# Performance work log

Hardware: AMD Instinct MI355X
Metric: run time of the kernel (lower is better)

Reference implementation:

```python
import jax, jax.numpy as jnp
import numpy as np

B, M, N, D, C = 4, 256, 64, 512, 1024  # batch, frames, tokens, d_model, n_classes


def setup_inputs() -> dict:
    key = jax.random.key(0)
    ks = jax.random.split(key, 6)
    s = 1.0 / np.sqrt(D)
    return {
        "encoder_out": jax.random.normal(ks[0], (B, M, D), jnp.float32),
        "decoder_out": jax.random.normal(ks[1], (B, N, D), jnp.float32),
        "W1": jax.random.normal(ks[2], (D, 2 * D), jnp.float32) * s,  # torch Linear [out,in], in=joint_size=2*d_model
        "b1": jax.random.normal(ks[3], (D,), jnp.float32) * s,
        "W2": jax.random.normal(ks[4], (C, D), jnp.float32) * s,
        "b2": jax.random.normal(ks[5], (C,), jnp.float32) * s,
    }


def reference(encoder_out, decoder_out, W1, b1, W2, b2):
    # cat([enc, dec], -1) @ W1.T == enc @ W1[:, :D].T + dec @ W1[:, D:].T
    # so project each side separately, then broadcast-add (avoids the [B,M,N,2D] concat).
    d = encoder_out.shape[-1]
    proj_enc = jnp.einsum("bmd,kd->bmk", encoder_out, W1[:, :d])   # [B,M,D]
    proj_dec = jnp.einsum("bnd,kd->bnk", decoder_out, W1[:, d:])   # [B,N,D]
    hidden = jnp.tanh(proj_enc[:, :, None, :] + proj_dec[:, None, :, :] + b1)  # [B,M,N,D]
    logits = jnp.einsum("bmnd,cd->bmnc", hidden, W2) + b2          # [B,M,N,C]
    return jax.nn.log_softmax(logits, axis=-1)
```

## Files before the change

kernel.cpp:

```cpp
#include <hip/hip_runtime.h>
#include <hip/hip_bf16.h>
#include <stdint.h>


typedef __bf16         bf16x8 __attribute__((ext_vector_type(8)));
typedef float          f32x4  __attribute__((ext_vector_type(4)));
typedef float          f32x16 __attribute__((ext_vector_type(16)));
typedef unsigned short u16x8  __attribute__((ext_vector_type(8)));

__device__ __forceinline__ unsigned short f2bf(float f) {
  unsigned int u = __float_as_uint(f);
  u += 0x7fffu + ((u >> 16) & 1u);
  return (unsigned short)(u >> 16);
}

__device__ __forceinline__ f32x4 mfma16(u16x8 a, u16x8 b, f32x4 c) {
  return __builtin_amdgcn_mfma_f32_16x16x32_bf16(
      __builtin_bit_cast(bf16x8, a), __builtin_bit_cast(bf16x8, b), c, 0, 0, 0);
}
__device__ __forceinline__ f32x16 mfma32(u16x8 a, u16x8 b, f32x16 c) {
  return __builtin_amdgcn_mfma_f32_32x32x16_bf16(
      __builtin_bit_cast(bf16x8, a), __builtin_bit_cast(bf16x8, b), c, 0, 0, 0);
}

__device__ __forceinline__ void stage16(const void* g, void* l) {
  __builtin_amdgcn_global_load_lds(
      (const __attribute__((address_space(1))) void*)g,
      (__attribute__((address_space(3))) void*)l, 16, 0, 0);
}

__global__ __launch_bounds__(256) void prep_kernel(
    const float* __restrict__ enc, const float* __restrict__ dec,
    const float* __restrict__ W1,  const float* __restrict__ W2,
    unsigned short* __restrict__ encB, unsigned short* __restrict__ decB,
    unsigned short* __restrict__ W1eB, unsigned short* __restrict__ W1dB,
    unsigned short* __restrict__ W2t)
{
  const int i = blockIdx.x * 256 + threadIdx.x;
  encB[i] = f2bf(enc[i]);
  {
    const int e  = i & 7;
    const int l  = (i >> 3) & 63;
    const int cb = (i >> 9) & 1;
    const int ks = (i >> 10) & 31;
    const int w  = i >> 15;
    const int col = w * 64 + cb * 32 + (l & 31);
    const int k   = ks * 16 + (l >> 5) * 8 + e;
    W2t[i] = f2bf(W2[col * 512 + k]);
  }
  if (i < 262144) {
    const int k = i >> 9, d = i & 511;
    W1eB[i] = f2bf(W1[k * 1024 + d]);
    W1dB[i] = f2bf(W1[k * 1024 + 512 + d]);
  }
  if (i < 131072) decB[i] = f2bf(dec[i]);
}

__global__ __launch_bounds__(256) void proj_kernel(
    const unsigned short* __restrict__ encB, const unsigned short* __restrict__ decB,
    const unsigned short* __restrict__ W1eB, const unsigned short* __restrict__ W1dB,
    const float* __restrict__ b1, float* __restrict__ pe, float* __restrict__ pd)
{
  int bid = blockIdx.x;
  const unsigned short *A, *Wt;
  const float* bias;
  float* out;
  if (bid < 128) { A = encB; Wt = W1eB; bias = nullptr; out = pe; }
  else           { bid -= 128; A = decB; Wt = W1dB; bias = b1; out = pd; }
  const int rtile = bid >> 3;
  const int ctile = bid & 7;
  const int w = threadIdx.x >> 6;
  const int l = threadIdx.x & 63;
  const int q = l >> 4, ln = l & 15;

  f32x4 acc[4] = {};
  const unsigned short* Ab = A  + (size_t)(rtile * 64 + ln) * 512 + q * 8;
  const unsigned short* Wb = Wt + (size_t)(ctile * 64 + w * 16 + ln) * 512 + q * 8;

#pragma unroll 4
  for (int ks = 0; ks < 16; ++ks) {
    u16x8 bv = *(const u16x8*)(Wb + ks * 32);
#pragma unroll
    for (int rf = 0; rf < 4; ++rf) {
      u16x8 av = *(const u16x8*)(Ab + rf * 16 * 512 + ks * 32);
      acc[rf] = mfma16(av, bv, acc[rf]);
    }
  }
  const int col = ctile * 64 + w * 16 + ln;
  const float bv = bias ? bias[col] : 0.0f;
#pragma unroll
  for (int rf = 0; rf < 4; ++rf)
#pragma unroll
    for (int j = 0; j < 4; ++j)
      out[(size_t)(rtile * 64 + rf * 16 + q * 4 + j) * 512 + col] = acc[rf][j] + bv;
}

__global__ __launch_bounds__(1024) void joint_kernel(
    const float* __restrict__ pe, const float* __restrict__ pd,
    const unsigned short* __restrict__ W2t, const float* __restrict__ b2,
    float* __restrict__ out)
{
  __shared__ unsigned short A_sh[64 * 512];
  __shared__ unsigned short B_sh[16 * 2048];
  __shared__ float red[64][17];
  __shared__ float lse_sh[64];

  const int blk = blockIdx.x;
  const int b   = blk >> 8;
  const int tid = threadIdx.x;
  const int w = tid >> 6, l = tid & 63;
  const int lo = l & 31, hi = l >> 5;

  const unsigned short* Wsrc = W2t + (size_t)w * 32768;
  unsigned short* Bdst = B_sh + w * 2048;

  stage16(Wsrc + l * 8,       Bdst);
  stage16(Wsrc + 512 + l * 8, Bdst + 512);

  float b2v[2];
#pragma unroll
  for (int cb = 0; cb < 2; ++cb) b2v[cb] = b2[w * 64 + cb * 32 + lo];
  asm volatile("" :: "v"(b2v[0]), "v"(b2v[1]));

  {
    const float* per = pe + (size_t)blk * 512 + l * 8;
    const float4 pe0 = *(const float4*)(per);
    const float4 pe1 = *(const float4*)(per + 4);
#pragma unroll
    for (int r = 0; r < 4; ++r) {
      const int n = (w << 2) | r;
      const float* pdr = pd + (size_t)((b << 6) | n) * 512 + l * 8;
      const float4 q0 = *(const float4*)(pdr);
      const float4 q1 = *(const float4*)(pdr + 4);
      float x[8] = {pe0.x + q0.x, pe0.y + q0.y, pe0.z + q0.z, pe0.w + q0.w,
                    pe1.x + q1.x, pe1.y + q1.y, pe1.z + q1.z, pe1.w + q1.w};
      u16x8 pk;
#pragma unroll
      for (int e = 0; e < 8; ++e) {
        const float ex = __expf(2.0f * x[e]);
        const float tv = 1.0f - 2.0f * __builtin_amdgcn_rcpf(ex + 1.0f);
        pk[e] = f2bf(tv);
      }
      *(u16x8*)((char*)A_sh + n * 1024 + ((l ^ (n & 7)) << 4)) = pk;
    }
  }
  __syncthreads();

  f32x16 acc[2][2];
#pragma unroll
  for (int rb = 0; rb < 2; ++rb)
#pragma unroll
    for (int cb = 0; cb < 2; ++cb) acc[rb][cb] = (f32x16)(0.f);

  const char* Abase = (const char*)A_sh + lo * 1024;
  const int x7 = lo & 7;
  const unsigned short* Bread = B_sh + w * 2048 + l * 8;

#pragma unroll
  for (int ks = 0; ks < 32; ++ks) {
    __builtin_amdgcn_sched_barrier(0);
    if (ks < 31) {
      stage16(Wsrc + (ks + 1) * 1024 + l * 8,       Bdst + ((ks + 1) & 1) * 1024);
      stage16(Wsrc + (ks + 1) * 1024 + 512 + l * 8, Bdst + ((ks + 1) & 1) * 1024 + 512);
      __builtin_amdgcn_sched_barrier(0);
      asm volatile("s_waitcnt vmcnt(2)" ::: "memory");
    } else {
      asm volatile("s_waitcnt vmcnt(0)" ::: "memory");
    }
    __builtin_amdgcn_sched_barrier(0);

    u16x8 bv[2], av[2];
#pragma unroll
    for (int cb = 0; cb < 2; ++cb)
      bv[cb] = *(const u16x8*)(Bread + (ks & 1) * 1024 + cb * 512);
#pragma unroll
    for (int rb = 0; rb < 2; ++rb)
      av[rb] = *(const u16x8*)(Abase + rb * 32768 + (((2 * ks + hi) ^ x7) << 4));
#pragma unroll
    for (int rb = 0; rb < 2; ++rb)
#pragma unroll
      for (int cb = 0; cb < 2; ++cb)
        acc[rb][cb] = mfma32(av[rb], bv[cb], acc[rb][cb]);
  }

  const float L2E = 1.4426950408889634f;
  const float LN2 = 0.6931471805599453f;

#pragma unroll
  for (int rb = 0; rb < 2; ++rb) {
    float s[16];
#pragma unroll
    for (int reg = 0; reg < 16; ++reg) {
      const float x0 = acc[rb][0][reg] + b2v[0];
      const float x1 = acc[rb][1][reg] + b2v[1];
      acc[rb][0][reg] = x0;
      acc[rb][1][reg] = x1;
      s[reg] = __builtin_amdgcn_exp2f(x0 * L2E) + __builtin_amdgcn_exp2f(x1 * L2E);
    }
#pragma unroll
    for (int o = 1; o < 32; o <<= 1)
#pragma unroll
      for (int reg = 0; reg < 16; ++reg)
        s[reg] += __shfl_xor(s[reg], o);
    if (lo == 0) {
#pragma unroll
      for (int reg = 0; reg < 16; ++reg) {
        const int row = rb * 32 + (reg & 3) + 8 * (reg >> 2) + 4 * hi;
        red[row][w] = s[reg];
      }
    }
  }
  __syncthreads();

  if (tid < 64) {
    float s = red[tid][0];
#pragma unroll
    for (int ww = 1; ww < 16; ++ww) s += red[tid][ww];
    lse_sh[tid] = LN2 * __builtin_amdgcn_logf(s);
  }
  __syncthreads();

  float* outb = out + (size_t)blk * 65536 + w * 64 + lo;
#pragma unroll
  for (int rb = 0; rb < 2; ++rb)
#pragma unroll
    for (int reg = 0; reg < 16; ++reg) {
      const int row = rb * 32 + (reg & 3) + 8 * (reg >> 2) + 4 * hi;
      const float lse = lse_sh[row];
      float* orow = outb + (size_t)row * 1024;
      orow[0]  = acc[rb][0][reg] - lse;
      orow[32] = acc[rb][1][reg] - lse;
    }
}

extern "C" void kernel_launch(void* const* d_in, const int* in_sizes, int n_in,
                              void* d_out, int out_size, void* d_ws, size_t ws_size,
                              hipStream_t stream) {
  (void)in_sizes; (void)n_in; (void)out_size; (void)ws_size;
  const float* enc = (const float*)d_in[0];
  const float* dec = (const float*)d_in[1];
  const float* W1  = (const float*)d_in[2];
  const float* b1  = (const float*)d_in[3];
  const float* W2  = (const float*)d_in[4];
  const float* b2  = (const float*)d_in[5];
  float* out = (float*)d_out;

  char* ws = (char*)d_ws;
  unsigned short* encB = (unsigned short*)(ws + 0);
  unsigned short* decB = (unsigned short*)(ws + 1048576);
  unsigned short* W1eB = (unsigned short*)(ws + 1310720);
  unsigned short* W1dB = (unsigned short*)(ws + 1835008);
  unsigned short* W2t  = (unsigned short*)(ws + 2359296);
  float*          pe   = (float*)(ws + 3407872);
  float*          pd   = (float*)(ws + 5505024);

  prep_kernel<<<2048, 256, 0, stream>>>(enc, dec, W1, W2, encB, decB, W1eB, W1dB, W2t);
  proj_kernel<<<160, 256, 0, stream>>>(encB, decB, W1eB, W1dB, b1, pe, pd);
  joint_kernel<<<1024, 1024, 0, stream>>>(pe, pd, W2t, b2, out);
}
```

Baseline: 152.0 us.

## Fuse bf16 prep conversion into projection kernel and drop intermediate buffers

Merges the prep and projection kernels into one launch. Projection blocks now read fp32 encoder, decoder and W1 directly and convert to bf16 in registers. Extra blocks in the same grid build the W2 transposed bf16 layout. This removes one kernel launch and the round trip through bf16 copies of enc, dec and W1. In exchange the projection reads twice the bytes per operand and repeats the conversion per tile, and the fp32 loads are less vectorized.

```diff
diff --git a/kernel.cpp b/kernel.cpp
--- a/kernel.cpp
+++ b/kernel.cpp
@@ -14,6 +14,15 @@
   return (unsigned short)(u >> 16);
 }
 
+__device__ __forceinline__ u16x8 cvt8(const float* p) {
+  const float4 a = *(const float4*)p;
+  const float4 b = *(const float4*)(p + 4);
+  u16x8 r;
+  r[0] = f2bf(a.x); r[1] = f2bf(a.y); r[2] = f2bf(a.z); r[3] = f2bf(a.w);
+  r[4] = f2bf(b.x); r[5] = f2bf(b.y); r[6] = f2bf(b.z); r[7] = f2bf(b.w);
+  return r;
+}
+
 __device__ __forceinline__ f32x4 mfma16(u16x8 a, u16x8 b, f32x4 c) {
   return __builtin_amdgcn_mfma_f32_16x16x32_bf16(
       __builtin_bit_cast(bf16x8, a), __builtin_bit_cast(bf16x8, b), c, 0, 0, 0);
@@ -29,60 +38,52 @@
       (__attribute__((address_space(3))) void*)l, 16, 0, 0);
 }
 
-__global__ __launch_bounds__(256) void prep_kernel(
+__global__ __launch_bounds__(256) void prep_proj_kernel(
     const float* __restrict__ enc, const float* __restrict__ dec,
     const float* __restrict__ W1,  const float* __restrict__ W2,
-    unsigned short* __restrict__ encB, unsigned short* __restrict__ decB,
-    unsigned short* __restrict__ W1eB, unsigned short* __restrict__ W1dB,
-    unsigned short* __restrict__ W2t)
+    const float* __restrict__ b1,
+    unsigned short* __restrict__ W2t, float* __restrict__ pe, float* __restrict__ pd)
 {
-  const int i = blockIdx.x * 256 + threadIdx.x;
-  encB[i] = f2bf(enc[i]);
-  {
-    const int e  = i & 7;
-    const int l  = (i >> 3) & 63;
-    const int cb = (i >> 9) & 1;
-    const int ks = (i >> 10) & 31;
-    const int w  = i >> 15;
-    const int col = w * 64 + cb * 32 + (l & 31);
-    const int k   = ks * 16 + (l >> 5) * 8 + e;
-    W2t[i] = f2bf(W2[col * 512 + k]);
-  }
-  if (i < 262144) {
-    const int k = i >> 9, d = i & 511;
-    W1eB[i] = f2bf(W1[k * 1024 + d]);
-    W1dB[i] = f2bf(W1[k * 1024 + 512 + d]);
-  }
-  if (i < 131072) decB[i] = f2bf(dec[i]);
-}
-
-__global__ __launch_bounds__(256) void proj_kernel(
-    const unsigned short* __restrict__ encB, const unsigned short* __restrict__ decB,
-    const unsigned short* __restrict__ W1eB, const unsigned short* __restrict__ W1dB,
-    const float* __restrict__ b1, float* __restrict__ pe, float* __restrict__ pd)
-{
-  int bid = blockIdx.x;
-  const unsigned short *A, *Wt;
+  const int bid = blockIdx.x;
+  if (bid >= 160) {
+    const int base = (bid - 160) * 4096;
+#pragma unroll
+    for (int j = 0; j < 16; ++j) {
+      const int i = base + j * 256 + threadIdx.x;
+      const int e  = i & 7;
+      const int l  = (i >> 3) & 63;
+      const int cb = (i >> 9) & 1;
+      const int ks = (i >> 10) & 31;
+      const int w  = i >> 15;
+      const int col = w * 64 + cb * 32 + (l & 31);
+      const int k   = ks * 16 + (l >> 5) * 8 + e;
+      W2t[i] = f2bf(W2[col * 512 + k]);
+    }
+    return;
+  }
+
+  int pb = bid;
+  const float* Af;
   const float* bias;
-  float* out;
-  if (bid < 128) { A = encB; Wt = W1eB; bias = nullptr; out = pe; }
-  else           { bid -= 128; A = decB; Wt = W1dB; bias = b1; out = pd; }
-  const int rtile = bid >> 3;
-  const int ctile = bid & 7;
+  float* outp;
+  int woff;
+  if (pb < 128) { Af = enc; bias = nullptr; outp = pe; woff = 0; }
+  else { pb -= 128; Af = dec; bias = b1; outp = pd; woff = 512; }
+  const int rtile = pb >> 3;
+  const int ctile = pb & 7;
   const int w = threadIdx.x >> 6;
   const int l = threadIdx.x & 63;
   const int q = l >> 4, ln = l & 15;
 
   f32x4 acc[4] = {};
-  const unsigned short* Ab = A  + (size_t)(rtile * 64 + ln) * 512 + q * 8;
-  const unsigned short* Wb = Wt + (size_t)(ctile * 64 + w * 16 + ln) * 512 + q * 8;
-
-#pragma unroll 4
+  const float* Ab = Af + (size_t)(rtile * 64 + ln) * 512 + q * 8;
+  const float* Wb = W1 + (size_t)(ctile * 64 + w * 16 + ln) * 1024 + woff + q * 8;
+
   for (int ks = 0; ks < 16; ++ks) {
-    u16x8 bv = *(const u16x8*)(Wb + ks * 32);
+    u16x8 bv = cvt8(Wb + ks * 32);
 #pragma unroll
     for (int rf = 0; rf < 4; ++rf) {
-      u16x8 av = *(const u16x8*)(Ab + rf * 16 * 512 + ks * 32);
+      u16x8 av = cvt8(Ab + rf * 16 * 512 + ks * 32);
       acc[rf] = mfma16(av, bv, acc[rf]);
     }
   }
@@ -92,7 +93,7 @@
   for (int rf = 0; rf < 4; ++rf)
 #pragma unroll
     for (int j = 0; j < 4; ++j)
-      out[(size_t)(rtile * 64 + rf * 16 + q * 4 + j) * 512 + col] = acc[rf][j] + bv;
+      outp[(size_t)(rtile * 64 + rf * 16 + q * 4 + j) * 512 + col] = acc[rf][j] + bv;
 }
 
 __global__ __launch_bounds__(1024) void joint_kernel(
@@ -246,15 +247,10 @@
   float* out = (float*)d_out;
 
   char* ws = (char*)d_ws;
-  unsigned short* encB = (unsigned short*)(ws + 0);
-  unsigned short* decB = (unsigned short*)(ws + 1048576);
-  unsigned short* W1eB = (unsigned short*)(ws + 1310720);
-  unsigned short* W1dB = (unsigned short*)(ws + 1835008);
-  unsigned short* W2t  = (unsigned short*)(ws + 2359296);
-  float*          pe   = (float*)(ws + 3407872);
-  float*          pd   = (float*)(ws + 5505024);
-
-  prep_kernel<<<2048, 256, 0, stream>>>(enc, dec, W1, W2, encB, decB, W1eB, W1dB, W2t);
-  proj_kernel<<<160, 256, 0, stream>>>(encB, decB, W1eB, W1dB, b1, pe, pd);
+  unsigned short* W2t = (unsigned short*)(ws + 0);
+  float*          pe  = (float*)(ws + 1048576);
+  float*          pd  = (float*)(ws + 3145728);
+
+  prep_proj_kernel<<<288, 256, 0, stream>>>(enc, dec, W1, W2, b1, W2t, pe, pd);
   joint_kernel<<<1024, 1024, 0, stream>>>(pe, pd, W2t, b2, out);
 }
```

Result: no change. 154.4 us (+1.6%).
